# Kernel optimization log

Measured on AMD Instinct MI355X. Metric: run time of the kernel, lower is better.

Reference implementation:

```python
import jax, jax.numpy as jnp
import numpy as np

NUM_HEADS = 4
HEAD_DIM = 64  # out_dim // num_heads = 256 // 4
NEG_SLOPE = 0.2


def setup_inputs() -> dict:
    key = jax.random.key(0)
    k1, k2 = jax.random.split(key)
    h = jax.random.normal(k1, (8, 2048, 256), dtype=jnp.float32)
    # Linear(in_dim, head_dim*num_heads, bias=False): store as [in_dim, out_dim]
    W = jax.random.normal(k2, (256, 256), dtype=jnp.float32) * (1.0 / np.sqrt(256.0))
    return {"h": h, "W": W}


def reference(h, W):
    B, T, _ = h.shape
    # Wh: (B, H, T, D)
    Wh = (h @ W).reshape(B, T, NUM_HEADS, HEAD_DIM).transpose(0, 2, 1, 3)
    scale = 1.0 / (HEAD_DIM ** 0.5)
    # full T x T scores per head, LeakyReLU then softmax over keys
    scores = jnp.einsum('bhtd,bhsd->bhts', Wh, Wh) * scale
    attention = jax.nn.softmax(jax.nn.leaky_relu(scores, negative_slope=NEG_SLOPE), axis=-1)
    h_prime = jnp.einsum('bhts,bhsd->bhtd', attention, Wh)
    # concat=True: (B, T, H*D)
    return h_prime.transpose(0, 2, 1, 3).reshape(B, T, NUM_HEADS * HEAD_DIM)
```

## Files before the change

### kernel.cpp

```cpp
#include <hip/hip_runtime.h>

#define T_SEQ 2048
#define NH 4
#define DH 64

typedef __bf16 bf16x8 __attribute__((ext_vector_type(8)));
typedef float f32x4 __attribute__((ext_vector_type(4)));

__device__ __forceinline__ unsigned short f2bf_rne(float x) {
  unsigned int u = __builtin_bit_cast(unsigned int, x);
  u += 0x7fffu + ((u >> 16) & 1u);
  return (unsigned short)(u >> 16);
}

__device__ __forceinline__ void async_cp16(const unsigned short* g, unsigned short* l) {
  __builtin_amdgcn_global_load_lds(
      (const __attribute__((address_space(1))) unsigned int*)g,
      (__attribute__((address_space(3))) unsigned int*)l, 16, 0, 0);
}

__global__ __launch_bounds__(256, 2) void wh_gemm(
    const float* __restrict__ h, const float* __restrict__ W,
    unsigned short* __restrict__ Kb, unsigned short* __restrict__ Vt) {
  __shared__ __align__(16) float hs[32 * 256];
  const int tid = threadIdx.x;
  const int mbase = blockIdx.x * 32;
  const float4* hblk = (const float4*)(h + (size_t)mbase * 256);
#pragma unroll
  for (int i = 0; i < 8; i++) {
    int slot = i * 256 + tid;
    ((float4*)hs)[slot] = hblk[slot];
  }
  __syncthreads();
  const int nid = tid & 63;
  const int rg = tid >> 6;
  float acc[8][4];
#pragma unroll
  for (int r = 0; r < 8; r++)
#pragma unroll
    for (int j = 0; j < 4; j++) acc[r][j] = 0.f;
  const float4* Wv = (const float4*)W;
  for (int k = 0; k < 256; k += 2) {
    float4 w0 = Wv[k * 64 + nid];
    float4 w1 = Wv[(k + 1) * 64 + nid];
#pragma unroll
    for (int r = 0; r < 8; r++) {
      float2 hv = *(const float2*)&hs[(rg * 8 + r) * 256 + k];
      acc[r][0] += hv.x * w0.x; acc[r][1] += hv.x * w0.y;
      acc[r][2] += hv.x * w0.z; acc[r][3] += hv.x * w0.w;
      acc[r][0] += hv.y * w1.x; acc[r][1] += hv.y * w1.y;
      acc[r][2] += hv.y * w1.z; acc[r][3] += hv.y * w1.w;
    }
  }
  const float s1 = 0.424664717f;
  const int head = nid >> 4;
  const int d0 = (nid & 15) * 4;
#pragma unroll
  for (int r = 0; r < 8; r++) {
    int m = mbase + rg * 8 + r;
    int b = m >> 11, t = m & 2047;
    size_t bh = (size_t)(b * NH + head);
    ushort4 kp;
    kp.x = f2bf_rne(acc[r][0] * s1);
    kp.y = f2bf_rne(acc[r][1] * s1);
    kp.z = f2bf_rne(acc[r][2] * s1);
    kp.w = f2bf_rne(acc[r][3] * s1);
    *(ushort4*)&Kb[(bh * T_SEQ + t) * DH + d0] = kp;
    size_t vtb = (bh * DH + d0) * T_SEQ + t;
    Vt[vtb]             = f2bf_rne(acc[r][0]);
    Vt[vtb + T_SEQ]     = f2bf_rne(acc[r][1]);
    Vt[vtb + 2 * T_SEQ] = f2bf_rne(acc[r][2]);
    Vt[vtb + 3 * T_SEQ] = f2bf_rne(acc[r][3]);
  }
}

__global__ __launch_bounds__(256, 4) void attn(
    const unsigned short* __restrict__ Kb, const unsigned short* __restrict__ Vt,
    float* __restrict__ out) {
  __shared__ __align__(16) unsigned short ldsK[64 * 64];
  __shared__ __align__(16) unsigned short ldsV[64 * 64];
  __shared__ __align__(16) unsigned short ldsP[4][16 * 64];
  const int tid = threadIdx.x;
  const int wave = tid >> 6;
  const int lane = tid & 63;
  const int l15 = lane & 15;
  const int quad = lane >> 4;
  const int bh = blockIdx.x >> 5;
  const int qtile = blockIdx.x & 31;
  const unsigned short* Kbh = Kb + (size_t)bh * T_SEQ * DH;
  const unsigned short* Vbh = Vt + (size_t)bh * DH * T_SEQ;

  const int qrow = qtile * 64 + wave * 16 + l15;
  bf16x8 aq0 = *(const bf16x8*)&Kbh[qrow * DH + quad * 8];
  bf16x8 aq1 = *(const bf16x8*)&Kbh[qrow * DH + 32 + quad * 8];

  f32x4 o[4];
  float lsum[4];
#pragma unroll
  for (int i = 0; i < 4; i++) {
    o[i] = (f32x4){0.f, 0.f, 0.f, 0.f};
    lsum[i] = 0.f;
  }
  unsigned short* Pw = ldsP[wave];

  for (int kt = 0; kt < 32; kt++) {
    __syncthreads();
#pragma unroll
    for (int i = 0; i < 2; i++) {
      int slot = i * 256 + tid;
      int r = slot >> 3;
      int c = (slot & 7) ^ (r & 7);
      unsigned short* lb = &ldsK[(i * 256 + wave * 64) * 8];
      async_cp16(&Kbh[(kt * 64 + r) * DH + c * 8], lb);
      unsigned short* lbv = &ldsV[(i * 256 + wave * 64) * 8];
      async_cp16(&Vbh[(size_t)r * T_SEQ + kt * 64 + c * 8], lbv);
    }
    __syncthreads();

    f32x4 sfr[4];
#pragma unroll
    for (int nt = 0; nt < 4; nt++) {
      int key = nt * 16 + l15;
      bf16x8 kf0 = *(const bf16x8*)&ldsK[key * 64 + ((quad ^ (key & 7)) << 3)];
      bf16x8 kf1 = *(const bf16x8*)&ldsK[key * 64 + (((4 + quad) ^ (key & 7)) << 3)];
      f32x4 s = {0.f, 0.f, 0.f, 0.f};
      s = __builtin_amdgcn_mfma_f32_16x16x32_bf16(aq0, kf0, s, 0, 0, 0);
      s = __builtin_amdgcn_mfma_f32_16x16x32_bf16(aq1, kf1, s, 0, 0, 0);
      sfr[nt] = s;
    }

#pragma unroll
    for (int nt = 0; nt < 4; nt++) {
      int col = nt * 16 + l15;
#pragma unroll
      for (int reg = 0; reg < 4; reg++) {
        float v = sfr[nt][reg];
        float e = __builtin_amdgcn_exp2f(fmaxf(v, 0.2f * v));
        lsum[reg] += e;
        int row = quad * 4 + reg;
        Pw[(row << 6) + (((((col >> 3) ^ (row & 7))) << 3) | (col & 7))] =
            (unsigned short)(__builtin_bit_cast(unsigned int, e) >> 16);
      }
    }
    __builtin_amdgcn_s_waitcnt(0xC07F);

#pragma unroll
    for (int kc = 0; kc < 2; kc++) {
      bf16x8 ap = *(const bf16x8*)&Pw[(l15 << 6) + ((((kc << 2) + quad) ^ (l15 & 7)) << 3)];
#pragma unroll
      for (int nt = 0; nt < 4; nt++) {
        int d = nt * 16 + l15;
        bf16x8 vf = *(const bf16x8*)&ldsV[(d << 6) + ((((kc << 2) + quad) ^ (d & 7)) << 3)];
        o[nt] = __builtin_amdgcn_mfma_f32_16x16x32_bf16(ap, vf, o[nt], 0, 0, 0);
      }
    }
  }

  float inv[4];
#pragma unroll
  for (int reg = 0; reg < 4; reg++) {
    float l = lsum[reg];
    l += __shfl_xor(l, 1, 64);
    l += __shfl_xor(l, 2, 64);
    l += __shfl_xor(l, 4, 64);
    l += __shfl_xor(l, 8, 64);
    inv[reg] = 1.0f / l;
  }
  const int b = bh >> 2, head = bh & 3;
#pragma unroll
  for (int nt = 0; nt < 4; nt++) {
    int d = nt * 16 + l15;
#pragma unroll
    for (int reg = 0; reg < 4; reg++) {
      int trow = qtile * 64 + wave * 16 + quad * 4 + reg;
      out[((size_t)b * T_SEQ + trow) * 256 + head * 64 + d] = o[nt][reg] * inv[reg];
    }
  }
}

extern "C" void kernel_launch(void* const* d_in, const int* in_sizes, int n_in,
                              void* d_out, int out_size, void* d_ws, size_t ws_size,
                              hipStream_t stream) {
  const float* h = (const float*)d_in[0];
  const float* W = (const float*)d_in[1];
  float* out = (float*)d_out;
  unsigned short* Kb = (unsigned short*)d_ws;
  unsigned short* Vt = Kb + (size_t)32 * T_SEQ * DH;
  wh_gemm<<<512, 256, 0, stream>>>(h, W, Kb, Vt);
  attn<<<32 * 32, 256, 0, stream>>>(Kb, Vt, out);
}
```

Baseline: 160.5 us.

## Rewrite projection GEMM on split-bf16 MFMA and restructure attention with register-held fragments

Adds a prep kernel that transposes W and splits it into bf16 hi/lo halves, stored temporarily in the output buffer. The projection GEMM now runs on MFMA using three-term split-bf16 products instead of scalar FP32 FMAs, and stages K and V^T through shared memory so global writes are coalesced. The attention kernel changes tiling: each wave handles 64 queries, loads K/V fragments straight from global into registers with double buffering instead of staging them in LDS, and drops block-level syncs. Occupancy falls to 1 block per CU with 256 blocks, and the split-bf16 GEMM carries some precision risk.

```diff
diff --git a/kernel.cpp b/kernel.cpp
--- a/kernel.cpp
+++ b/kernel.cpp
@@ -6,174 +6,236 @@
 
 typedef __bf16 bf16x8 __attribute__((ext_vector_type(8)));
 typedef float f32x4 __attribute__((ext_vector_type(4)));
+typedef unsigned short u16x8 __attribute__((ext_vector_type(8)));
 
 __device__ __forceinline__ unsigned short f2bf_rne(float x) {
   unsigned int u = __builtin_bit_cast(unsigned int, x);
   u += 0x7fffu + ((u >> 16) & 1u);
   return (unsigned short)(u >> 16);
 }
-
-__device__ __forceinline__ void async_cp16(const unsigned short* g, unsigned short* l) {
-  __builtin_amdgcn_global_load_lds(
-      (const __attribute__((address_space(1))) unsigned int*)g,
-      (__attribute__((address_space(3))) unsigned int*)l, 16, 0, 0);
+__device__ __forceinline__ float bf2f(unsigned short s) {
+  unsigned int u = ((unsigned int)s) << 16;
+  return __builtin_bit_cast(float, u);
+}
+
+__global__ void prep_w(const float* __restrict__ W,
+                       unsigned short* __restrict__ WtHi,
+                       unsigned short* __restrict__ WtLo) {
+  __shared__ float ls[32][65];
+  const int tid = threadIdx.x;
+  const int k0 = (blockIdx.x >> 2) * 32;
+  const int n0 = (blockIdx.x & 3) * 64;
+#pragma unroll
+  for (int i = 0; i < 8; i++) {
+    int e = i * 256 + tid;
+    int r = e >> 6, c = e & 63;
+    ls[r][c] = W[(k0 + r) * 256 + n0 + c];
+  }
+  __syncthreads();
+  const int n = tid & 63;
+  const int part = tid >> 6;
+  u16x8 vh, vl;
+#pragma unroll
+  for (int j = 0; j < 8; j++) {
+    float w = ls[part * 8 + j][n];
+    unsigned short h16 = f2bf_rne(w);
+    vh[j] = h16;
+    vl[j] = f2bf_rne(w - bf2f(h16));
+  }
+  size_t dst = (size_t)(n0 + n) * 256 + k0 + part * 8;
+  *(u16x8*)&WtHi[dst] = vh;
+  *(u16x8*)&WtLo[dst] = vl;
 }
 
 __global__ __launch_bounds__(256, 2) void wh_gemm(
-    const float* __restrict__ h, const float* __restrict__ W,
+    const float* __restrict__ h,
+    const unsigned short* __restrict__ WtHi,
+    const unsigned short* __restrict__ WtLo,
     unsigned short* __restrict__ Kb, unsigned short* __restrict__ Vt) {
-  __shared__ __align__(16) float hs[32 * 256];
+  __shared__ __align__(16) unsigned short ktile[32][264];
+  __shared__ __align__(16) unsigned short vtile[256][40];
   const int tid = threadIdx.x;
-  const int mbase = blockIdx.x * 32;
-  const float4* hblk = (const float4*)(h + (size_t)mbase * 256);
-#pragma unroll
-  for (int i = 0; i < 8; i++) {
-    int slot = i * 256 + tid;
-    ((float4*)hs)[slot] = hblk[slot];
+  const int wave = tid >> 6, lane = tid & 63, l15 = lane & 15, quad = lane >> 4;
+  const int m0b = blockIdx.x * 32;
+  const int m0 = m0b + (wave & 1) * 16;
+  const int n0w = (wave >> 1) * 128;
+  f32x4 acc[8];
+#pragma unroll
+  for (int nt = 0; nt < 8; nt++) acc[nt] = (f32x4){0.f, 0.f, 0.f, 0.f};
+
+  for (int kc = 0; kc < 8; kc++) {
+    const float4* hp = (const float4*)&h[(size_t)(m0 + l15) * 256 + kc * 32 + quad * 8];
+    float4 a0 = hp[0], a1 = hp[1];
+    float xs[8] = {a0.x, a0.y, a0.z, a0.w, a1.x, a1.y, a1.z, a1.w};
+    u16x8 ah, al;
+#pragma unroll
+    for (int j = 0; j < 8; j++) {
+      unsigned short h16 = f2bf_rne(xs[j]);
+      ah[j] = h16;
+      al[j] = f2bf_rne(xs[j] - bf2f(h16));
+    }
+    bf16x8 ahi = __builtin_bit_cast(bf16x8, ah);
+    bf16x8 alo = __builtin_bit_cast(bf16x8, al);
+#pragma unroll
+    for (int nt = 0; nt < 8; nt++) {
+      size_t wb = (size_t)(n0w + nt * 16 + l15) * 256 + kc * 32 + quad * 8;
+      bf16x8 bhi = *(const bf16x8*)&WtHi[wb];
+      bf16x8 blo = *(const bf16x8*)&WtLo[wb];
+      acc[nt] = __builtin_amdgcn_mfma_f32_16x16x32_bf16(ahi, bhi, acc[nt], 0, 0, 0);
+      acc[nt] = __builtin_amdgcn_mfma_f32_16x16x32_bf16(alo, bhi, acc[nt], 0, 0, 0);
+      acc[nt] = __builtin_amdgcn_mfma_f32_16x16x32_bf16(ahi, blo, acc[nt], 0, 0, 0);
+    }
+  }
+  const float s1 = 0.424664717f;
+  const int tl = (wave & 1) * 16 + quad * 4;
+#pragma unroll
+  for (int nt = 0; nt < 8; nt++) {
+    int n = n0w + nt * 16 + l15;
+#pragma unroll
+    for (int r = 0; r < 4; r++) {
+      float v = acc[nt][r];
+      ktile[tl + r][n] = f2bf_rne(v * s1);
+      vtile[n][tl + r] = f2bf_rne(v);
+    }
   }
   __syncthreads();
-  const int nid = tid & 63;
-  const int rg = tid >> 6;
-  float acc[8][4];
-#pragma unroll
-  for (int r = 0; r < 8; r++)
-#pragma unroll
-    for (int j = 0; j < 4; j++) acc[r][j] = 0.f;
-  const float4* Wv = (const float4*)W;
-  for (int k = 0; k < 256; k += 2) {
-    float4 w0 = Wv[k * 64 + nid];
-    float4 w1 = Wv[(k + 1) * 64 + nid];
-#pragma unroll
-    for (int r = 0; r < 8; r++) {
-      float2 hv = *(const float2*)&hs[(rg * 8 + r) * 256 + k];
-      acc[r][0] += hv.x * w0.x; acc[r][1] += hv.x * w0.y;
-      acc[r][2] += hv.x * w0.z; acc[r][3] += hv.x * w0.w;
-      acc[r][0] += hv.y * w1.x; acc[r][1] += hv.y * w1.y;
-      acc[r][2] += hv.y * w1.z; acc[r][3] += hv.y * w1.w;
-    }
-  }
-  const float s1 = 0.424664717f;
-  const int head = nid >> 4;
-  const int d0 = (nid & 15) * 4;
-#pragma unroll
-  for (int r = 0; r < 8; r++) {
-    int m = mbase + rg * 8 + r;
-    int b = m >> 11, t = m & 2047;
-    size_t bh = (size_t)(b * NH + head);
-    ushort4 kp;
-    kp.x = f2bf_rne(acc[r][0] * s1);
-    kp.y = f2bf_rne(acc[r][1] * s1);
-    kp.z = f2bf_rne(acc[r][2] * s1);
-    kp.w = f2bf_rne(acc[r][3] * s1);
-    *(ushort4*)&Kb[(bh * T_SEQ + t) * DH + d0] = kp;
-    size_t vtb = (bh * DH + d0) * T_SEQ + t;
-    Vt[vtb]             = f2bf_rne(acc[r][0]);
-    Vt[vtb + T_SEQ]     = f2bf_rne(acc[r][1]);
-    Vt[vtb + 2 * T_SEQ] = f2bf_rne(acc[r][2]);
-    Vt[vtb + 3 * T_SEQ] = f2bf_rne(acc[r][3]);
-  }
-}
-
-__global__ __launch_bounds__(256, 4) void attn(
+  {
+    int t = tid >> 3, seg = tid & 7;
+    int m = m0b + t, b = m >> 11, tt = m & 2047;
+    int head = seg >> 1, d0 = (seg & 1) * 32;
+    unsigned short* dst = &Kb[((size_t)(b * NH + head) * T_SEQ + tt) * DH + d0];
+#pragma unroll
+    for (int q = 0; q < 4; q++)
+      *(u16x8*)&dst[q * 8] = *(const u16x8*)&ktile[t][seg * 32 + q * 8];
+  }
+  {
+    int n = tid, head = n >> 6, d = n & 63;
+    int b = m0b >> 11, t0 = m0b & 2047;
+    unsigned short* dst = &Vt[((size_t)(b * NH + head) * DH + d) * T_SEQ + t0];
+#pragma unroll
+    for (int q = 0; q < 4; q++)
+      *(u16x8*)&dst[q * 8] = *(const u16x8*)&vtile[n][q * 8];
+  }
+}
+
+struct Frag {
+  bf16x8 k[2][2];
+  bf16x8 v[4];
+};
+
+__device__ __forceinline__ void load_frags(Frag& f, const unsigned short* Kbh,
+                                           const unsigned short* Vbh, int s0,
+                                           int l15, int quad) {
+#pragma unroll
+  for (int mt = 0; mt < 2; mt++)
+#pragma unroll
+    for (int kc = 0; kc < 2; kc++)
+      f.k[mt][kc] = *(const bf16x8*)&Kbh[(size_t)(s0 + mt * 16 + l15) * DH + kc * 32 + quad * 8];
+#pragma unroll
+  for (int dt = 0; dt < 4; dt++)
+    f.v[dt] = *(const bf16x8*)&Vbh[(size_t)(dt * 16 + l15) * T_SEQ + s0 + quad * 8];
+}
+
+__device__ __forceinline__ void step(const Frag& f, const bf16x8 bq[4][2],
+                                     f32x4 o[4][4], float* lsum,
+                                     unsigned short* Pw, int l15, int quad) {
+  f32x4 s[2][4];
+#pragma unroll
+  for (int mt = 0; mt < 2; mt++)
+#pragma unroll
+    for (int nt = 0; nt < 4; nt++) {
+      f32x4 c = {0.f, 0.f, 0.f, 0.f};
+      c = __builtin_amdgcn_mfma_f32_16x16x32_bf16(f.k[mt][0], bq[nt][0], c, 0, 0, 0);
+      c = __builtin_amdgcn_mfma_f32_16x16x32_bf16(f.k[mt][1], bq[nt][1], c, 0, 0, 0);
+      s[mt][nt] = c;
+    }
+#pragma unroll
+  for (int mt = 0; mt < 2; mt++)
+#pragma unroll
+    for (int nt = 0; nt < 4; nt++) {
+      float e0, e1, e2, e3;
+      {
+        float v0 = s[mt][nt][0], v1 = s[mt][nt][1];
+        float v2 = s[mt][nt][2], v3 = s[mt][nt][3];
+        e0 = __builtin_amdgcn_exp2f(fmaxf(v0, 0.2f * v0));
+        e1 = __builtin_amdgcn_exp2f(fmaxf(v1, 0.2f * v1));
+        e2 = __builtin_amdgcn_exp2f(fmaxf(v2, 0.2f * v2));
+        e3 = __builtin_amdgcn_exp2f(fmaxf(v3, 0.2f * v3));
+      }
+      lsum[nt] += (e0 + e1) + (e2 + e3);
+      uint2 pk;
+      pk.x = (__builtin_bit_cast(unsigned int, e1) & 0xffff0000u) |
+             (__builtin_bit_cast(unsigned int, e0) >> 16);
+      pk.y = (__builtin_bit_cast(unsigned int, e3) & 0xffff0000u) |
+             (__builtin_bit_cast(unsigned int, e2) >> 16);
+      *(uint2*)&Pw[(nt * 16 + l15) * 40 + mt * 16 + quad * 4] = pk;
+    }
+  __builtin_amdgcn_s_waitcnt(0xC07F);
+#pragma unroll
+  for (int mt = 0; mt < 4; mt++) {
+    bf16x8 pa = *(const bf16x8*)&Pw[(mt * 16 + l15) * 40 + quad * 8];
+#pragma unroll
+    for (int dt = 0; dt < 4; dt++)
+      o[mt][dt] = __builtin_amdgcn_mfma_f32_16x16x32_bf16(pa, f.v[dt], o[mt][dt], 0, 0, 0);
+  }
+}
+
+__global__ __launch_bounds__(256, 1) void attn(
     const unsigned short* __restrict__ Kb, const unsigned short* __restrict__ Vt,
     float* __restrict__ out) {
-  __shared__ __align__(16) unsigned short ldsK[64 * 64];
-  __shared__ __align__(16) unsigned short ldsV[64 * 64];
-  __shared__ __align__(16) unsigned short ldsP[4][16 * 64];
-  const int tid = threadIdx.x;
-  const int wave = tid >> 6;
-  const int lane = tid & 63;
-  const int l15 = lane & 15;
-  const int quad = lane >> 4;
-  const int bh = blockIdx.x >> 5;
-  const int qtile = blockIdx.x & 31;
+  __shared__ __align__(16) unsigned short Pw_all[4][64 * 40];
+  __shared__ float inv_lds[4][64];
+  const int tid = threadIdx.x, wave = tid >> 6, lane = tid & 63;
+  const int l15 = lane & 15, quad = lane >> 4;
+  const int bh = blockIdx.x & 31;
+  const int qt = blockIdx.x >> 5;
+  const int q0 = qt * 256 + wave * 64;
   const unsigned short* Kbh = Kb + (size_t)bh * T_SEQ * DH;
   const unsigned short* Vbh = Vt + (size_t)bh * DH * T_SEQ;
-
-  const int qrow = qtile * 64 + wave * 16 + l15;
-  bf16x8 aq0 = *(const bf16x8*)&Kbh[qrow * DH + quad * 8];
-  bf16x8 aq1 = *(const bf16x8*)&Kbh[qrow * DH + 32 + quad * 8];
-
-  f32x4 o[4];
-  float lsum[4];
-#pragma unroll
-  for (int i = 0; i < 4; i++) {
-    o[i] = (f32x4){0.f, 0.f, 0.f, 0.f};
-    lsum[i] = 0.f;
-  }
-  unsigned short* Pw = ldsP[wave];
-
-  for (int kt = 0; kt < 32; kt++) {
-    __syncthreads();
-#pragma unroll
-    for (int i = 0; i < 2; i++) {
-      int slot = i * 256 + tid;
-      int r = slot >> 3;
-      int c = (slot & 7) ^ (r & 7);
-      unsigned short* lb = &ldsK[(i * 256 + wave * 64) * 8];
-      async_cp16(&Kbh[(kt * 64 + r) * DH + c * 8], lb);
-      unsigned short* lbv = &ldsV[(i * 256 + wave * 64) * 8];
-      async_cp16(&Vbh[(size_t)r * T_SEQ + kt * 64 + c * 8], lbv);
-    }
-    __syncthreads();
-
-    f32x4 sfr[4];
-#pragma unroll
-    for (int nt = 0; nt < 4; nt++) {
-      int key = nt * 16 + l15;
-      bf16x8 kf0 = *(const bf16x8*)&ldsK[key * 64 + ((quad ^ (key & 7)) << 3)];
-      bf16x8 kf1 = *(const bf16x8*)&ldsK[key * 64 + (((4 + quad) ^ (key & 7)) << 3)];
-      f32x4 s = {0.f, 0.f, 0.f, 0.f};
-      s = __builtin_amdgcn_mfma_f32_16x16x32_bf16(aq0, kf0, s, 0, 0, 0);
-      s = __builtin_amdgcn_mfma_f32_16x16x32_bf16(aq1, kf1, s, 0, 0, 0);
-      sfr[nt] = s;
-    }
-
-#pragma unroll
-    for (int nt = 0; nt < 4; nt++) {
-      int col = nt * 16 + l15;
-#pragma unroll
-      for (int reg = 0; reg < 4; reg++) {
-        float v = sfr[nt][reg];
-        float e = __builtin_amdgcn_exp2f(fmaxf(v, 0.2f * v));
-        lsum[reg] += e;
-        int row = quad * 4 + reg;
-        Pw[(row << 6) + (((((col >> 3) ^ (row & 7))) << 3) | (col & 7))] =
-            (unsigned short)(__builtin_bit_cast(unsigned int, e) >> 16);
-      }
-    }
-    __builtin_amdgcn_s_waitcnt(0xC07F);
-
-#pragma unroll
-    for (int kc = 0; kc < 2; kc++) {
-      bf16x8 ap = *(const bf16x8*)&Pw[(l15 << 6) + ((((kc << 2) + quad) ^ (l15 & 7)) << 3)];
-#pragma unroll
-      for (int nt = 0; nt < 4; nt++) {
-        int d = nt * 16 + l15;
-        bf16x8 vf = *(const bf16x8*)&ldsV[(d << 6) + ((((kc << 2) + quad) ^ (d & 7)) << 3)];
-        o[nt] = __builtin_amdgcn_mfma_f32_16x16x32_bf16(ap, vf, o[nt], 0, 0, 0);
-      }
-    }
-  }
-
-  float inv[4];
-#pragma unroll
-  for (int reg = 0; reg < 4; reg++) {
-    float l = lsum[reg];
-    l += __shfl_xor(l, 1, 64);
-    l += __shfl_xor(l, 2, 64);
-    l += __shfl_xor(l, 4, 64);
-    l += __shfl_xor(l, 8, 64);
-    inv[reg] = 1.0f / l;
-  }
+  unsigned short* Pw = Pw_all[wave];
+
+  bf16x8 bq[4][2];
+#pragma unroll
+  for (int nt = 0; nt < 4; nt++)
+#pragma unroll
+    for (int kc = 0; kc < 2; kc++)
+      bq[nt][kc] = *(const bf16x8*)&Kbh[(size_t)(q0 + nt * 16 + l15) * DH + kc * 32 + quad * 8];
+
+  f32x4 o[4][4];
+  float lsum[4] = {0.f, 0.f, 0.f, 0.f};
+#pragma unroll
+  for (int mt = 0; mt < 4; mt++)
+#pragma unroll
+    for (int dt = 0; dt < 4; dt++) o[mt][dt] = (f32x4){0.f, 0.f, 0.f, 0.f};
+
+  Frag fa, fb;
+  load_frags(fa, Kbh, Vbh, 0, l15, quad);
+  for (int it = 0; it < 64; it += 2) {
+    load_frags(fb, Kbh, Vbh, (it + 1) * 32, l15, quad);
+    step(fa, bq, o, lsum, Pw, l15, quad);
+    load_frags(fa, Kbh, Vbh, (it + 2 < 64) ? (it + 2) * 32 : 0, l15, quad);
+    step(fb, bq, o, lsum, Pw, l15, quad);
+  }
+
+#pragma unroll
+  for (int nt = 0; nt < 4; nt++) {
+    float l = lsum[nt];
+    l += __shfl_xor(l, 16, 64);
+    l += __shfl_xor(l, 32, 64);
+    if (quad == 0) inv_lds[wave][nt * 16 + l15] = 1.0f / l;
+  }
+  __builtin_amdgcn_s_waitcnt(0xC07F);
+
   const int b = bh >> 2, head = bh & 3;
 #pragma unroll
-  for (int nt = 0; nt < 4; nt++) {
-    int d = nt * 16 + l15;
-#pragma unroll
-    for (int reg = 0; reg < 4; reg++) {
-      int trow = qtile * 64 + wave * 16 + quad * 4 + reg;
-      out[((size_t)b * T_SEQ + trow) * 256 + head * 64 + d] = o[nt][reg] * inv[reg];
+  for (int mt = 0; mt < 4; mt++) {
+#pragma unroll
+    for (int r = 0; r < 4; r++) {
+      float iv = inv_lds[wave][mt * 16 + quad * 4 + r];
+      int qg = q0 + mt * 16 + quad * 4 + r;
+      float* dst = &out[((size_t)b * T_SEQ + qg) * 256 + head * DH];
+#pragma unroll
+      for (int dt = 0; dt < 4; dt++) dst[dt * 16 + l15] = o[mt][dt][r] * iv;
     }
   }
 }
@@ -186,6 +248,9 @@
   float* out = (float*)d_out;
   unsigned short* Kb = (unsigned short*)d_ws;
   unsigned short* Vt = Kb + (size_t)32 * T_SEQ * DH;
-  wh_gemm<<<512, 256, 0, stream>>>(h, W, Kb, Vt);
-  attn<<<32 * 32, 256, 0, stream>>>(Kb, Vt, out);
-}
+  unsigned short* WtHi = (unsigned short*)out;
+  unsigned short* WtLo = WtHi + 65536;
+  prep_w<<<32, 256, 0, stream>>>(W, WtHi, WtLo);
+  wh_gemm<<<512, 256, 0, stream>>>(h, WtHi, WtLo, Kb, Vt);
+  attn<<<256, 256, 0, stream>>>(Kb, Vt, out);
+}
```

Result: slower. 171.5 us (+6.8%).
